# Kernel tuning notes

Measured on AMD Instinct MI355X. Metric: run time of the kernel, lower is better.

## Reference

```python
import jax, jax.numpy as jnp
import numpy as np

N = 500_000      # number of gaussians
F = 32           # grid feature dim (WavePlaneField.feat_dim)
R = 128          # plane resolution
W = 256          # MLP width
BOUNDS = 1.6     # scene aabb half-extent (args.bounds)


def setup_inputs() -> dict:
    key = jax.random.key(0)
    ks = jax.random.split(key, 16)
    s = lambda d: 1.0 / np.sqrt(d)
    return {
        "rays_pts_emb": jax.random.normal(ks[0], (N, 3), jnp.float32),
        "rotations_emb": jax.random.normal(ks[1], (N, 4), jnp.float32),
        "scale_emb": jax.random.uniform(ks[2], (N, 3), jnp.float32),
        "shs_emb": jax.random.normal(ks[3], (N, 16, 3), jnp.float32),
        "view_dir": jax.random.normal(ks[4], (N, 3), jnp.float32),
        "time_emb": jax.random.uniform(ks[5], (N, 1), jnp.float32),
        "h_emb": jax.random.normal(ks[6], (N, 2), jnp.float32),
        # multiplicative k-planes: init near 1 so products are well-scaled
        "space_planes": 1.0 + 0.1 * jax.random.normal(ks[7], (3, R, R, F), jnp.float32),
        "time_planes": 1.0 + 0.1 * jax.random.normal(ks[8], (3, R, R, F), jnp.float32),
        "w_enc": s(F) * jax.random.normal(ks[9], (F, W), jnp.float32),
        "b_enc": jnp.zeros((W,), jnp.float32),
        "w1": s(W) * jax.random.normal(ks[10], (W, W), jnp.float32),
        "b1": jnp.zeros((W,), jnp.float32),
        "w2": s(W) * jax.random.normal(ks[11], (W, 16 * 3), jnp.float32),
        "b2": jnp.zeros((16 * 3,), jnp.float32),
    }


def _interp2d(plane, u, v):
    """Bilinear sample plane [R,R,F] at normalized coords u,v in [0,1]. -> [N,F]"""
    Rr = plane.shape[0]
    x = jnp.clip(u, 0.0, 1.0) * (Rr - 1)
    y = jnp.clip(v, 0.0, 1.0) * (Rr - 1)
    x0 = jnp.clip(jnp.floor(x), 0, Rr - 2).astype(jnp.int32)
    y0 = jnp.clip(jnp.floor(y), 0, Rr - 2).astype(jnp.int32)
    fx = (x - x0)[:, None]
    fy = (y - y0)[:, None]
    p00 = plane[y0, x0]
    p01 = plane[y0, x0 + 1]
    p10 = plane[y0 + 1, x0]
    p11 = plane[y0 + 1, x0 + 1]
    return (p00 * (1 - fx) + p01 * fx) * (1 - fy) + (p10 * (1 - fx) + p11 * fx) * fy


def _covariance(scale, rotation):
    """3DGS: L = R(q) @ diag(s); cov = L L^T; return 6 unique entries [N,6]."""
    q = rotation / jnp.linalg.norm(rotation, axis=-1, keepdims=True)
    r, x, y, z = q[:, 0], q[:, 1], q[:, 2], q[:, 3]
    Rm = jnp.stack([
        jnp.stack([1 - 2 * (y * y + z * z), 2 * (x * y - r * z), 2 * (x * z + r * y)], -1),
        jnp.stack([2 * (x * y + r * z), 1 - 2 * (x * x + z * z), 2 * (y * z - r * x)], -1),
        jnp.stack([2 * (x * z - r * y), 2 * (y * z + r * x), 1 - 2 * (x * x + y * y)], -1),
    ], axis=1)  # [N,3,3]
    L = Rm * scale[:, None, :]                      # R @ diag(s)
    cov = jnp.einsum('nij,nkj->nik', L, L)          # L @ L^T
    return jnp.stack([cov[:, 0, 0], cov[:, 0, 1], cov[:, 0, 2],
                      cov[:, 1, 1], cov[:, 1, 2], cov[:, 2, 2]], axis=-1)


def reference(rays_pts_emb, rotations_emb, scale_emb, shs_emb, view_dir, time_emb,
              h_emb, space_planes, time_planes, w_enc, b_enc, w1, b1, w2, b2):
    # quaternion -> covariance (passed into grid in original; grid lookup itself
    # only needs positions/time, so symm is computed but unused downstream)
    symm = _covariance(scale_emb, rotations_emb)

    pts = rays_pts_emb[:, :3]
    pn = jnp.clip(pts / BOUNDS, -1.0, 1.0) * 0.5 + 0.5  # aabb-normalize to [0,1]
    xn, yn, zn = pn[:, 0], pn[:, 1], pn[:, 2]
    t = jnp.clip(time_emb[:, 0], 0.0, 1.0)

    space = (_interp2d(space_planes[0], xn, yn)
             * _interp2d(space_planes[1], xn, zn)
             * _interp2d(space_planes[2], yn, zn))          # [N,F]
    spacetime = (_interp2d(time_planes[0], xn, t)
                 * _interp2d(time_planes[1], yn, t)
                 * _interp2d(time_planes[2], zn, t))        # [N,F]

    feat = (space * spacetime) @ w_enc + b_enc              # spacetime_enc (Linear only)
    h = jax.nn.relu(feat) @ w1 + b1                         # shs_deform MLP
    d = jax.nn.relu(h) @ w2 + b2                            # [N,48]
    shs = shs_emb + d.reshape(-1, 16, 3)

    del symm  # original forward discards covariance after grid query
    return (rays_pts_emb, rotations_emb, h_emb[:, 0:1], shs)
```

## Files before the change

### kernel.cpp

```cpp
#include <hip/hip_runtime.h>
#include <hip/hip_fp16.h>

#define NPTS 500000
#define RPLANE 128
#define FDIM 32
#define PLSZ (RPLANE * RPLANE * FDIM)
#define NTILES 15625
#define NBLK 977
#define TSTRIDE (NBLK * 8)

typedef __bf16 bfx8 __attribute__((ext_vector_type(8)));
typedef float f32x4 __attribute__((ext_vector_type(4)));

__device__ __forceinline__ unsigned short f2bf(float f) {
    unsigned int u = __builtin_bit_cast(unsigned int, f);
    unsigned int r = (u + 0x7FFFu + ((u >> 16) & 1u)) >> 16;
    return (unsigned short)r;
}

__device__ __forceinline__ unsigned pk2(float a, float b) {
    return (unsigned)f2bf(a) | ((unsigned)f2bf(b) << 16);
}

__device__ __forceinline__ __half2 u2h(unsigned u) {
    return __builtin_bit_cast(__half2, u);
}

__device__ __forceinline__ bfx8 asfrag(uint4 v) {
    return __builtin_bit_cast(bfx8, v);
}

__device__ __forceinline__ uint4 convD(unsigned e0, unsigned e1, unsigned o0,
                                       unsigned o1, int a0, int a1, bool sel) {
    uint4 W;
    int x, y;
    x = __builtin_amdgcn_ds_bpermute(a0, (int)e0);
    y = __builtin_amdgcn_ds_bpermute(a0, (int)o0);
    W.x = (unsigned)(sel ? y : x);
    x = __builtin_amdgcn_ds_bpermute(a0, (int)e1);
    y = __builtin_amdgcn_ds_bpermute(a0, (int)o1);
    W.y = (unsigned)(sel ? y : x);
    x = __builtin_amdgcn_ds_bpermute(a1, (int)e0);
    y = __builtin_amdgcn_ds_bpermute(a1, (int)o0);
    W.z = (unsigned)(sel ? y : x);
    x = __builtin_amdgcn_ds_bpermute(a1, (int)e1);
    y = __builtin_amdgcn_ds_bpermute(a1, (int)o1);
    W.w = (unsigned)(sel ? y : x);
    return W;
}

__global__ void prep_all(const float* __restrict__ wenc, const float* __restrict__ w1,
                         const float* __restrict__ w2, const float* __restrict__ spf,
                         const float* __restrict__ tpf,
                         unsigned short* __restrict__ wf, __half* __restrict__ ph) {
    const int WTOT = 86016;
    const int PTOT = 6 * PLSZ;
    const int total = WTOT + PTOT;
    for (int i = blockIdx.x * blockDim.x + threadIdx.x; i < total;
         i += gridDim.x * blockDim.x) {
        if (i < WTOT) {
            const float* W;
            unsigned short* dst;
            int K, Ncols, idx;
            if (i < 8192)       { W = wenc; K = 32;  Ncols = 256; idx = i;         dst = wf; }
            else if (i < 73728) { W = w1;   K = 256; Ncols = 256; idx = i - 8192;  dst = wf + 8192; }
            else                { W = w2;   K = 256; Ncols = 48;  idx = i - 73728; dst = wf + 73728; }
            int j = idx & 7;
            int l = (idx >> 3) & 63;
            int b = idx >> 9;
            int KS = K >> 5;
            int ct = b / KS;
            int ks = b - ct * KS;
            int k = ks * 32 + ((l >> 4) << 3) + j;
            int col = ct * 16 + (l & 15);
            dst[idx] = f2bf(W[(size_t)k * Ncols + col]);
        } else {
            int j = i - WTOT;
            float v = (j < 3 * PLSZ) ? spf[j] : tpf[j - 3 * PLSZ];
            ph[j] = __float2half(v);
        }
    }
}

__global__ void pass_copy(const float* __restrict__ rays, const float* __restrict__ rot,
                          const float* __restrict__ h, float* __restrict__ out) {
    const int total = NPTS * 8;
    for (int i = blockIdx.x * blockDim.x + threadIdx.x; i < total; i += gridDim.x * blockDim.x) {
        float v;
        if (i < NPTS * 3) v = rays[i];
        else if (i < NPTS * 7) v = rot[i - NPTS * 3];
        else v = h[(i - NPTS * 7) * 2];
        out[i] = v;
    }
}

__global__ __launch_bounds__(512, 2) void fused5(
    const float* __restrict__ rays, const float* __restrict__ tme,
    const float* __restrict__ shs, const __half* __restrict__ ph,
    const unsigned short* __restrict__ wf,
    const float* __restrict__ benc, const float* __restrict__ b1v,
    const float* __restrict__ b2v, float* __restrict__ out) {
    __shared__ unsigned short wlds[77824];
    const int tid = threadIdx.x;
    const int wid = tid >> 6;
    const int lane = tid & 63;

#pragma unroll
    for (int i = tid * 8; i < 77824; i += 512 * 8)
        *(uint4*)&wlds[i] = *(const uint4*)(wf + 8192 + i);
    __syncthreads();

    const int g = lane >> 4;
    const int c = lane & 15;
    const int f0 = g << 3;
    const int a0 = 4 * (32 * (g & 1) + c);
    const int a1 = a0 + 64;
    const bool sel = (g >> 1) != 0;

    for (int k = 0; k < 2; ++k) {
        int tile = blockIdx.x * 8 + wid + k * TSTRIDE;
        if (tile >= NTILES) continue;
        const int p0 = tile * 32;

        bfx8 act1[2];
#pragma unroll
        for (int pt = 0; pt < 2; ++pt) {
            int p = p0 + pt * 16 + c;
            float px = rays[p * 3 + 0], py = rays[p * 3 + 1], pz = rays[p * 3 + 2];
            const float inv = 0.625f;
            float xn = fminf(fmaxf(px * inv, -1.f), 1.f) * 0.5f + 0.5f;
            float yn = fminf(fmaxf(py * inv, -1.f), 1.f) * 0.5f + 0.5f;
            float zn = fminf(fmaxf(pz * inv, -1.f), 1.f) * 0.5f + 0.5f;
            float tt = fminf(fmaxf(tme[p], 0.f), 1.f);
            float c4[4] = {xn, yn, zn, tt};
            int i0[4];
            float fr[4];
#pragma unroll
            for (int cc = 0; cc < 4; ++cc) {
                float x = c4[cc] * 127.0f;
                float xf = fminf(floorf(x), 126.0f);
                i0[cc] = (int)xf;
                fr[cc] = x - xf;
            }
            const int uc[6] = {0, 0, 1, 0, 1, 2};
            const int vc[6] = {1, 2, 2, 3, 3, 3};
            __half2 g2[4];
#pragma unroll
            for (int pl = 0; pl < 6; ++pl) {
                int x0 = i0[uc[pl]], y0 = i0[vc[pl]];
                float fx = fr[uc[pl]], fy = fr[vc[pl]];
                const __half* base = ph + (size_t)pl * PLSZ + ((y0 * RPLANE + x0) << 5) + f0;
                uint4 q00 = *(const uint4*)base;
                uint4 q01 = *(const uint4*)(base + FDIM);
                uint4 q10 = *(const uint4*)(base + RPLANE * FDIM);
                uint4 q11 = *(const uint4*)(base + RPLANE * FDIM + FDIM);
                __half2 wa = __float2half2_rn((1.f - fx) * (1.f - fy));
                __half2 wb = __float2half2_rn(fx * (1.f - fy));
                __half2 wc = __float2half2_rn((1.f - fx) * fy);
                __half2 wd = __float2half2_rn(fx * fy);
                unsigned qa[4] = {q00.x, q00.y, q00.z, q00.w};
                unsigned qb[4] = {q01.x, q01.y, q01.z, q01.w};
                unsigned qc[4] = {q10.x, q10.y, q10.z, q10.w};
                unsigned qd[4] = {q11.x, q11.y, q11.z, q11.w};
#pragma unroll
                for (int i = 0; i < 4; ++i) {
                    __half2 r = __hmul2(u2h(qa[i]), wa);
                    r = __hfma2(u2h(qb[i]), wb, r);
                    r = __hfma2(u2h(qc[i]), wc, r);
                    r = __hfma2(u2h(qd[i]), wd, r);
                    g2[i] = (pl == 0) ? r : __hmul2(g2[i], r);
                }
            }
            uint4 av;
            {
                float2 v0 = __half22float2(g2[0]);
                float2 v1 = __half22float2(g2[1]);
                float2 v2 = __half22float2(g2[2]);
                float2 v3 = __half22float2(g2[3]);
                av.x = pk2(v0.x, v0.y);
                av.y = pk2(v1.x, v1.y);
                av.z = pk2(v2.x, v2.y);
                av.w = pk2(v3.x, v3.y);
            }
            act1[pt] = asfrag(av);
        }

        uint4 act2[2][8];
        {
            unsigned stE[2][2];
#pragma unroll
            for (int ct = 0; ct < 16; ++ct) {
                uint4 cur = *(const uint4*)(wf + (size_t)ct * 512 + lane * 8);
                float4 b4 = *(const float4*)(benc + 16 * ct + 4 * g);
                float bb[4] = {b4.x, b4.y, b4.z, b4.w};
#pragma unroll
                for (int pt = 0; pt < 2; ++pt) {
                    f32x4 z = {0.f, 0.f, 0.f, 0.f};
                    f32x4 d = __builtin_amdgcn_mfma_f32_16x16x32_bf16(asfrag(cur), act1[pt], z, 0, 0, 0);
                    float v0 = fmaxf(d[0] + bb[0], 0.f);
                    float v1 = fmaxf(d[1] + bb[1], 0.f);
                    float v2 = fmaxf(d[2] + bb[2], 0.f);
                    float v3 = fmaxf(d[3] + bb[3], 0.f);
                    unsigned Q0 = pk2(v0, v1), Q1 = pk2(v2, v3);
                    if ((ct & 1) == 0) {
                        stE[pt][0] = Q0; stE[pt][1] = Q1;
                    } else {
                        act2[pt][ct >> 1] = convD(stE[pt][0], stE[pt][1], Q0, Q1, a0, a1, sel);
                    }
                }
            }
        }

        uint4 act3[2][8];
        {
            unsigned stE[2][2];
#pragma unroll
            for (int ct = 0; ct < 16; ++ct) {
                uint4 w[8];
#pragma unroll
                for (int ks = 0; ks < 8; ++ks)
                    w[ks] = *(const uint4*)&wlds[(ct * 8 + ks) * 512 + lane * 8];
                float4 b4 = *(const float4*)(b1v + 16 * ct + 4 * g);
                float bb[4] = {b4.x, b4.y, b4.z, b4.w};
#pragma unroll
                for (int pt = 0; pt < 2; ++pt) {
                    f32x4 acc = {0.f, 0.f, 0.f, 0.f};
#pragma unroll
                    for (int ks = 0; ks < 8; ++ks)
                        acc = __builtin_amdgcn_mfma_f32_16x16x32_bf16(asfrag(w[ks]), asfrag(act2[pt][ks]), acc, 0, 0, 0);
                    float v0 = fmaxf(acc[0] + bb[0], 0.f);
                    float v1 = fmaxf(acc[1] + bb[1], 0.f);
                    float v2 = fmaxf(acc[2] + bb[2], 0.f);
                    float v3 = fmaxf(acc[3] + bb[3], 0.f);
                    unsigned Q0 = pk2(v0, v1), Q1 = pk2(v2, v3);
                    if ((ct & 1) == 0) {
                        stE[pt][0] = Q0; stE[pt][1] = Q1;
                    } else {
                        act3[pt][ct >> 1] = convD(stE[pt][0], stE[pt][1], Q0, Q1, a0, a1, sel);
                    }
                }
            }
        }

        {
#pragma unroll
            for (int ct = 0; ct < 3; ++ct) {
                uint4 wl[8];
#pragma unroll
                for (int ks = 0; ks < 8; ++ks)
                    wl[ks] = *(const uint4*)&wlds[65536 + (ct * 8 + ks) * 512 + lane * 8];
                float bias = b2v[16 * ct + c];
#pragma unroll
                for (int pt = 0; pt < 2; ++pt) {
                    f32x4 acc = {0.f, 0.f, 0.f, 0.f};
#pragma unroll
                    for (int ks = 0; ks < 8; ++ks)
                        acc = __builtin_amdgcn_mfma_f32_16x16x32_bf16(asfrag(act3[pt][ks]), asfrag(wl[ks]), acc, 0, 0, 0);
#pragma unroll
                    for (int r = 0; r < 4; ++r) {
                        int p = p0 + pt * 16 + 4 * g + r;
                        size_t idx = (size_t)p * 48 + 16 * ct + c;
                        out[(size_t)NPTS * 8 + idx] = shs[idx] + acc[r] + bias;
                    }
                }
            }
        }
    }
}

extern "C" void kernel_launch(void* const* d_in, const int* in_sizes, int n_in,
                              void* d_out, int out_size, void* d_ws, size_t ws_size,
                              hipStream_t stream) {
    const float* rays = (const float*)d_in[0];
    const float* rot  = (const float*)d_in[1];
    const float* shs  = (const float*)d_in[3];
    const float* tme  = (const float*)d_in[5];
    const float* h_e  = (const float*)d_in[6];
    const float* spf  = (const float*)d_in[7];
    const float* tpf  = (const float*)d_in[8];
    const float* wenc = (const float*)d_in[9];
    const float* benc = (const float*)d_in[10];
    const float* w1   = (const float*)d_in[11];
    const float* b1v  = (const float*)d_in[12];
    const float* w2   = (const float*)d_in[13];
    const float* b2v  = (const float*)d_in[14];
    float* out = (float*)d_out;
    unsigned short* wf = (unsigned short*)d_ws;
    __half* ph = (__half*)(wf + 86016);

    prep_all<<<3408, 256, 0, stream>>>(wenc, w1, w2, spf, tpf, wf, ph);
    pass_copy<<<2048, 256, 0, stream>>>(rays, rot, h_e, out);
    fused5<<<NBLK, 512, 0, stream>>>(
        rays, tme, shs, ph, wf, benc, b1v, b2v, out);
}
```

Before: 207.3 us.

## Split plane gathering into separate kernel, stage features in output scratch

Moves the bilinear k-plane sampling out of the MFMA kernel into a per-point gather kernel that also performs the passthrough copies. The gathered features are written as bf16 fragments into the shs region of the output buffer, which the MLP kernel later overwrites. The MLP kernel then runs persistently with 256 blocks, launch bounds of 1 block per CU, and up to 8 tiles per wave, so the large weight load into LDS is done fewer times. The intent is to separate the latency-bound gather from MFMA work and reduce the per-block LDS weight fills. The cost is an extra global round trip of 32 bytes per point and lower occupancy in the MLP kernel.

```diff
diff --git a/kernel.cpp b/kernel.cpp
--- a/kernel.cpp
+++ b/kernel.cpp
@@ -6,8 +6,7 @@
 #define FDIM 32
 #define PLSZ (RPLANE * RPLANE * FDIM)
 #define NTILES 15625
-#define NBLK 977
-#define TSTRIDE (NBLK * 8)
+#define NWAVES 2048
 
 typedef __bf16 bfx8 __attribute__((ext_vector_type(8)));
 typedef float f32x4 __attribute__((ext_vector_type(4)));
@@ -82,29 +81,93 @@
     }
 }
 
-__global__ void pass_copy(const float* __restrict__ rays, const float* __restrict__ rot,
-                          const float* __restrict__ h, float* __restrict__ out) {
-    const int total = NPTS * 8;
-    for (int i = blockIdx.x * blockDim.x + threadIdx.x; i < total; i += gridDim.x * blockDim.x) {
-        float v;
-        if (i < NPTS * 3) v = rays[i];
-        else if (i < NPTS * 7) v = rot[i - NPTS * 3];
-        else v = h[(i - NPTS * 7) * 2];
-        out[i] = v;
-    }
-}
-
-__global__ __launch_bounds__(512, 2) void fused5(
-    const float* __restrict__ rays, const float* __restrict__ tme,
-    const float* __restrict__ shs, const __half* __restrict__ ph,
-    const unsigned short* __restrict__ wf,
+__global__ void gather_feat(const float* __restrict__ rays, const float* __restrict__ tme,
+                            const float* __restrict__ rot, const float* __restrict__ h_e,
+                            const __half* __restrict__ ph, float* __restrict__ out) {
+    int p = blockIdx.x * blockDim.x + threadIdx.x;
+    if (p >= NPTS) return;
+    float3 r3 = *(const float3*)(rays + 3 * p);
+    out[3 * p + 0] = r3.x;
+    out[3 * p + 1] = r3.y;
+    out[3 * p + 2] = r3.z;
+    float4 r4 = *(const float4*)(rot + 4 * p);
+    *(float4*)(out + 3 * NPTS + 4 * p) = r4;
+    out[7 * NPTS + p] = h_e[2 * p];
+
+    const float inv = 0.625f;
+    float xn = fminf(fmaxf(r3.x * inv, -1.f), 1.f) * 0.5f + 0.5f;
+    float yn = fminf(fmaxf(r3.y * inv, -1.f), 1.f) * 0.5f + 0.5f;
+    float zn = fminf(fmaxf(r3.z * inv, -1.f), 1.f) * 0.5f + 0.5f;
+    float tt = fminf(fmaxf(tme[p], 0.f), 1.f);
+    float c4[4] = {xn, yn, zn, tt};
+    int i0[4];
+    float fr[4];
+#pragma unroll
+    for (int cc = 0; cc < 4; ++cc) {
+        float x = c4[cc] * 127.0f;
+        float xf = fminf(floorf(x), 126.0f);
+        i0[cc] = (int)xf;
+        fr[cc] = x - xf;
+    }
+    const int uc[6] = {0, 0, 1, 0, 1, 2};
+    const int vc[6] = {1, 2, 2, 3, 3, 3};
+    __half2 g2[16];
+#pragma unroll
+    for (int pl = 0; pl < 6; ++pl) {
+        int x0 = i0[uc[pl]], y0 = i0[vc[pl]];
+        float fx = fr[uc[pl]], fy = fr[vc[pl]];
+        const __half* base = ph + (size_t)pl * PLSZ + ((y0 * RPLANE + x0) << 5);
+        const uint4* b00 = (const uint4*)base;
+        const uint4* b01 = (const uint4*)(base + FDIM);
+        const uint4* b10 = (const uint4*)(base + RPLANE * FDIM);
+        const uint4* b11 = (const uint4*)(base + RPLANE * FDIM + FDIM);
+        __half2 wa = __float2half2_rn((1.f - fx) * (1.f - fy));
+        __half2 wb = __float2half2_rn(fx * (1.f - fy));
+        __half2 wc = __float2half2_rn((1.f - fx) * fy);
+        __half2 wd = __float2half2_rn(fx * fy);
+#pragma unroll
+        for (int q = 0; q < 4; ++q) {
+            uint4 A = b00[q], B = b01[q], C = b10[q], D = b11[q];
+            unsigned ua[4] = {A.x, A.y, A.z, A.w};
+            unsigned ub[4] = {B.x, B.y, B.z, B.w};
+            unsigned uccr[4] = {C.x, C.y, C.z, C.w};
+            unsigned ud[4] = {D.x, D.y, D.z, D.w};
+#pragma unroll
+            for (int j = 0; j < 4; ++j) {
+                __half2 r = __hmul2(u2h(ua[j]), wa);
+                r = __hfma2(u2h(ub[j]), wb, r);
+                r = __hfma2(u2h(uccr[j]), wc, r);
+                r = __hfma2(u2h(ud[j]), wd, r);
+                int i = q * 4 + j;
+                g2[i] = (pl == 0) ? r : __hmul2(g2[i], r);
+            }
+        }
+    }
+    int f = p >> 4, c = p & 15;
+    char* fb = (char*)out + (size_t)NPTS * 32 + (size_t)f * 3072;
+#pragma unroll
+    for (int g = 0; g < 4; ++g) {
+        float2 v0 = __half22float2(g2[4 * g + 0]);
+        float2 v1 = __half22float2(g2[4 * g + 1]);
+        float2 v2 = __half22float2(g2[4 * g + 2]);
+        float2 v3 = __half22float2(g2[4 * g + 3]);
+        uint4 av;
+        av.x = pk2(v0.x, v0.y);
+        av.y = pk2(v1.x, v1.y);
+        av.z = pk2(v2.x, v2.y);
+        av.w = pk2(v3.x, v3.y);
+        *(uint4*)(fb + (g * 16 + c) * 16) = av;
+    }
+}
+
+__global__ __launch_bounds__(512, 1) void mlp6(
+    const float* __restrict__ shs, const unsigned short* __restrict__ wf,
     const float* __restrict__ benc, const float* __restrict__ b1v,
     const float* __restrict__ b2v, float* __restrict__ out) {
     __shared__ unsigned short wlds[77824];
     const int tid = threadIdx.x;
     const int wid = tid >> 6;
     const int lane = tid & 63;
-
 #pragma unroll
     for (int i = tid * 8; i < 77824; i += 512 * 8)
         *(uint4*)&wlds[i] = *(const uint4*)(wf + 8192 + i);
@@ -112,78 +175,20 @@
 
     const int g = lane >> 4;
     const int c = lane & 15;
-    const int f0 = g << 3;
     const int a0 = 4 * (32 * (g & 1) + c);
     const int a1 = a0 + 64;
     const bool sel = (g >> 1) != 0;
-
-    for (int k = 0; k < 2; ++k) {
-        int tile = blockIdx.x * 8 + wid + k * TSTRIDE;
-        if (tile >= NTILES) continue;
+    const char* fb = (const char*)out + (size_t)NPTS * 32;
+    const int w = blockIdx.x * 8 + wid;
+
+    for (int it = 0; it < 8; ++it) {
+        int tile = w + NWAVES * it;
+        if (tile >= NTILES) break;
         const int p0 = tile * 32;
 
         bfx8 act1[2];
-#pragma unroll
-        for (int pt = 0; pt < 2; ++pt) {
-            int p = p0 + pt * 16 + c;
-            float px = rays[p * 3 + 0], py = rays[p * 3 + 1], pz = rays[p * 3 + 2];
-            const float inv = 0.625f;
-            float xn = fminf(fmaxf(px * inv, -1.f), 1.f) * 0.5f + 0.5f;
-            float yn = fminf(fmaxf(py * inv, -1.f), 1.f) * 0.5f + 0.5f;
-            float zn = fminf(fmaxf(pz * inv, -1.f), 1.f) * 0.5f + 0.5f;
-            float tt = fminf(fmaxf(tme[p], 0.f), 1.f);
-            float c4[4] = {xn, yn, zn, tt};
-            int i0[4];
-            float fr[4];
-#pragma unroll
-            for (int cc = 0; cc < 4; ++cc) {
-                float x = c4[cc] * 127.0f;
-                float xf = fminf(floorf(x), 126.0f);
-                i0[cc] = (int)xf;
-                fr[cc] = x - xf;
-            }
-            const int uc[6] = {0, 0, 1, 0, 1, 2};
-            const int vc[6] = {1, 2, 2, 3, 3, 3};
-            __half2 g2[4];
-#pragma unroll
-            for (int pl = 0; pl < 6; ++pl) {
-                int x0 = i0[uc[pl]], y0 = i0[vc[pl]];
-                float fx = fr[uc[pl]], fy = fr[vc[pl]];
-                const __half* base = ph + (size_t)pl * PLSZ + ((y0 * RPLANE + x0) << 5) + f0;
-                uint4 q00 = *(const uint4*)base;
-                uint4 q01 = *(const uint4*)(base + FDIM);
-                uint4 q10 = *(const uint4*)(base + RPLANE * FDIM);
-                uint4 q11 = *(const uint4*)(base + RPLANE * FDIM + FDIM);
-                __half2 wa = __float2half2_rn((1.f - fx) * (1.f - fy));
-                __half2 wb = __float2half2_rn(fx * (1.f - fy));
-                __half2 wc = __float2half2_rn((1.f - fx) * fy);
-                __half2 wd = __float2half2_rn(fx * fy);
-                unsigned qa[4] = {q00.x, q00.y, q00.z, q00.w};
-                unsigned qb[4] = {q01.x, q01.y, q01.z, q01.w};
-                unsigned qc[4] = {q10.x, q10.y, q10.z, q10.w};
-                unsigned qd[4] = {q11.x, q11.y, q11.z, q11.w};
-#pragma unroll
-                for (int i = 0; i < 4; ++i) {
-                    __half2 r = __hmul2(u2h(qa[i]), wa);
-                    r = __hfma2(u2h(qb[i]), wb, r);
-                    r = __hfma2(u2h(qc[i]), wc, r);
-                    r = __hfma2(u2h(qd[i]), wd, r);
-                    g2[i] = (pl == 0) ? r : __hmul2(g2[i], r);
-                }
-            }
-            uint4 av;
-            {
-                float2 v0 = __half22float2(g2[0]);
-                float2 v1 = __half22float2(g2[1]);
-                float2 v2 = __half22float2(g2[2]);
-                float2 v3 = __half22float2(g2[3]);
-                av.x = pk2(v0.x, v0.y);
-                av.y = pk2(v1.x, v1.y);
-                av.z = pk2(v2.x, v2.y);
-                av.w = pk2(v3.x, v3.y);
-            }
-            act1[pt] = asfrag(av);
-        }
+        act1[0] = asfrag(*(const uint4*)(fb + (size_t)(2 * tile + 0) * 3072 + lane * 16));
+        act1[1] = asfrag(*(const uint4*)(fb + (size_t)(2 * tile + 1) * 3072 + lane * 16));
 
         uint4 act2[2][8];
         {
@@ -216,10 +221,10 @@
             unsigned stE[2][2];
 #pragma unroll
             for (int ct = 0; ct < 16; ++ct) {
-                uint4 w[8];
+                uint4 wv[8];
 #pragma unroll
                 for (int ks = 0; ks < 8; ++ks)
-                    w[ks] = *(const uint4*)&wlds[(ct * 8 + ks) * 512 + lane * 8];
+                    wv[ks] = *(const uint4*)&wlds[(ct * 8 + ks) * 512 + lane * 8];
                 float4 b4 = *(const float4*)(b1v + 16 * ct + 4 * g);
                 float bb[4] = {b4.x, b4.y, b4.z, b4.w};
 #pragma unroll
@@ -227,7 +232,7 @@
                     f32x4 acc = {0.f, 0.f, 0.f, 0.f};
 #pragma unroll
                     for (int ks = 0; ks < 8; ++ks)
-                        acc = __builtin_amdgcn_mfma_f32_16x16x32_bf16(asfrag(w[ks]), asfrag(act2[pt][ks]), acc, 0, 0, 0);
+                        acc = __builtin_amdgcn_mfma_f32_16x16x32_bf16(asfrag(wv[ks]), asfrag(act2[pt][ks]), acc, 0, 0, 0);
                     float v0 = fmaxf(acc[0] + bb[0], 0.f);
                     float v1 = fmaxf(acc[1] + bb[1], 0.f);
                     float v2 = fmaxf(acc[2] + bb[2], 0.f);
@@ -289,7 +294,6 @@
     __half* ph = (__half*)(wf + 86016);
 
     prep_all<<<3408, 256, 0, stream>>>(wenc, w1, w2, spf, tpf, wf, ph);
-    pass_copy<<<2048, 256, 0, stream>>>(rays, rot, h_e, out);
-    fused5<<<NBLK, 512, 0, stream>>>(
-        rays, tme, shs, ph, wf, benc, b1v, b2v, out);
-}
+    gather_feat<<<(NPTS + 255) / 256, 256, 0, stream>>>(rays, tme, rot, h_e, ph, out);
+    mlp6<<<256, 512, 0, stream>>>(shs, wf, benc, b1v, b2v, out);
+}
```

After: 263.8 us. +27.2%, slower.

## Fuse passthrough copy into main kernel and use persistent 256-block grid

Applied to the files above, without the earlier changes.

Removes the separate pass_copy kernel by copying rays, rotations and h for each tile inside the fused MLP kernel. The main kernel switches to a persistent grid of 256 blocks, each wave looping over up to 8 tiles, so the per-block LDS weight load is amortized over more tiles. The plane fp32-to-fp16 conversion is vectorized to handle two elements per thread with float2 loads. This saves a launch and some bandwidth passes, but the smaller grid may leave CUs underused or unbalanced across the 15625 tiles.

```diff
diff --git a/kernel.cpp b/kernel.cpp
--- a/kernel.cpp
+++ b/kernel.cpp
@@ -6,8 +6,7 @@
 #define FDIM 32
 #define PLSZ (RPLANE * RPLANE * FDIM)
 #define NTILES 15625
-#define NBLK 977
-#define TSTRIDE (NBLK * 8)
+#define NWAVES 2048
 
 typedef __bf16 bfx8 __attribute__((ext_vector_type(8)));
 typedef float f32x4 __attribute__((ext_vector_type(4)));
@@ -49,13 +48,13 @@
     return W;
 }
 
-__global__ void prep_all(const float* __restrict__ wenc, const float* __restrict__ w1,
-                         const float* __restrict__ w2, const float* __restrict__ spf,
-                         const float* __restrict__ tpf,
-                         unsigned short* __restrict__ wf, __half* __restrict__ ph) {
+__global__ void prep2(const float* __restrict__ wenc, const float* __restrict__ w1,
+                      const float* __restrict__ w2, const float* __restrict__ spf,
+                      const float* __restrict__ tpf,
+                      unsigned short* __restrict__ wf, __half* __restrict__ ph) {
     const int WTOT = 86016;
-    const int PTOT = 6 * PLSZ;
-    const int total = WTOT + PTOT;
+    const int PHALF = 3 * PLSZ;
+    const int total = WTOT + PHALF;
     for (int i = blockIdx.x * blockDim.x + threadIdx.x; i < total;
          i += gridDim.x * blockDim.x) {
         if (i < WTOT) {
@@ -75,27 +74,17 @@
             int col = ct * 16 + (l & 15);
             dst[idx] = f2bf(W[(size_t)k * Ncols + col]);
         } else {
-            int j = i - WTOT;
-            float v = (j < 3 * PLSZ) ? spf[j] : tpf[j - 3 * PLSZ];
-            ph[j] = __float2half(v);
+            int j2 = (i - WTOT) * 2;
+            const float* src = (j2 < 3 * PLSZ) ? spf + j2 : tpf + (j2 - 3 * PLSZ);
+            float2 v = *(const float2*)src;
+            *(__half2*)(ph + j2) = __floats2half2_rn(v.x, v.y);
         }
     }
 }
 
-__global__ void pass_copy(const float* __restrict__ rays, const float* __restrict__ rot,
-                          const float* __restrict__ h, float* __restrict__ out) {
-    const int total = NPTS * 8;
-    for (int i = blockIdx.x * blockDim.x + threadIdx.x; i < total; i += gridDim.x * blockDim.x) {
-        float v;
-        if (i < NPTS * 3) v = rays[i];
-        else if (i < NPTS * 7) v = rot[i - NPTS * 3];
-        else v = h[(i - NPTS * 7) * 2];
-        out[i] = v;
-    }
-}
-
-__global__ __launch_bounds__(512, 2) void fused5(
+__global__ __launch_bounds__(512, 2) void fused7(
     const float* __restrict__ rays, const float* __restrict__ tme,
+    const float* __restrict__ rot, const float* __restrict__ h_e,
     const float* __restrict__ shs, const __half* __restrict__ ph,
     const unsigned short* __restrict__ wf,
     const float* __restrict__ benc, const float* __restrict__ b1v,
@@ -112,15 +101,21 @@
 
     const int g = lane >> 4;
     const int c = lane & 15;
-    const int f0 = g << 3;
     const int a0 = 4 * (32 * (g & 1) + c);
     const int a1 = a0 + 64;
     const bool sel = (g >> 1) != 0;
-
-    for (int k = 0; k < 2; ++k) {
-        int tile = blockIdx.x * 8 + wid + k * TSTRIDE;
-        if (tile >= NTILES) continue;
+    const int w = blockIdx.x * 8 + wid;
+
+    for (int it = 0; it < 8; ++it) {
+        int tile = w + NWAVES * it;
+        if (tile >= NTILES) break;
         const int p0 = tile * 32;
+
+        out[3 * p0 + lane] = rays[3 * p0 + lane];
+        if (lane < 32) out[3 * p0 + 64 + lane] = rays[3 * p0 + 64 + lane];
+        out[3 * NPTS + 4 * p0 + lane] = rot[4 * p0 + lane];
+        out[3 * NPTS + 4 * p0 + 64 + lane] = rot[4 * p0 + 64 + lane];
+        if (lane < 32) out[7 * NPTS + p0 + lane] = h_e[2 * (p0 + lane)];
 
         bfx8 act1[2];
 #pragma unroll
@@ -149,7 +144,7 @@
             for (int pl = 0; pl < 6; ++pl) {
                 int x0 = i0[uc[pl]], y0 = i0[vc[pl]];
                 float fx = fr[uc[pl]], fy = fr[vc[pl]];
-                const __half* base = ph + (size_t)pl * PLSZ + ((y0 * RPLANE + x0) << 5) + f0;
+                const __half* base = ph + (size_t)pl * PLSZ + ((y0 * RPLANE + x0) << 5) + (g << 3);
                 uint4 q00 = *(const uint4*)base;
                 uint4 q01 = *(const uint4*)(base + FDIM);
                 uint4 q10 = *(const uint4*)(base + RPLANE * FDIM);
@@ -216,10 +211,10 @@
             unsigned stE[2][2];
 #pragma unroll
             for (int ct = 0; ct < 16; ++ct) {
-                uint4 w[8];
+                uint4 wv[8];
 #pragma unroll
                 for (int ks = 0; ks < 8; ++ks)
-                    w[ks] = *(const uint4*)&wlds[(ct * 8 + ks) * 512 + lane * 8];
+                    wv[ks] = *(const uint4*)&wlds[(ct * 8 + ks) * 512 + lane * 8];
                 float4 b4 = *(const float4*)(b1v + 16 * ct + 4 * g);
                 float bb[4] = {b4.x, b4.y, b4.z, b4.w};
 #pragma unroll
@@ -227,7 +222,7 @@
                     f32x4 acc = {0.f, 0.f, 0.f, 0.f};
 #pragma unroll
                     for (int ks = 0; ks < 8; ++ks)
-                        acc = __builtin_amdgcn_mfma_f32_16x16x32_bf16(asfrag(w[ks]), asfrag(act2[pt][ks]), acc, 0, 0, 0);
+                        acc = __builtin_amdgcn_mfma_f32_16x16x32_bf16(asfrag(wv[ks]), asfrag(act2[pt][ks]), acc, 0, 0, 0);
                     float v0 = fmaxf(acc[0] + bb[0], 0.f);
                     float v1 = fmaxf(acc[1] + bb[1], 0.f);
                     float v2 = fmaxf(acc[2] + bb[2], 0.f);
@@ -288,8 +283,7 @@
     unsigned short* wf = (unsigned short*)d_ws;
     __half* ph = (__half*)(wf + 86016);
 
-    prep_all<<<3408, 256, 0, stream>>>(wenc, w1, w2, spf, tpf, wf, ph);
-    pass_copy<<<2048, 256, 0, stream>>>(rays, rot, h_e, out);
-    fused5<<<NBLK, 512, 0, stream>>>(
-        rays, tme, shs, ph, wf, benc, b1v, b2v, out);
-}
+    prep2<<<2048, 256, 0, stream>>>(wenc, w1, w2, spf, tpf, wf, ph);
+    fused7<<<256, 512, 0, stream>>>(rays, tme, rot, h_e, shs, ph, wf,
+                                    benc, b1v, b2v, out);
+}
```

Result: slower. 240.6 us (+16.0%).
